# Performance work log

Measured on AMD Instinct MI355X. Metric: run time of the kernel, lower is better.

The kernel has to match this reference:

```python
import jax, jax.numpy as jnp
import numpy as np
from jax import lax

E = 8      # embed dim
H = 8      # num heads (head_dim = 1)
EPS = 1e-5


def pe_row(pos, d=E):
    # PositionalEncoding quirk: original adds pe[:, x.size(1), :] -> a SINGLE row at index L.
    i = jnp.arange(0, d, 2, dtype=jnp.float32)
    div = jnp.exp(i * (-np.log(10000.0) / d))
    row = jnp.zeros((d,), jnp.float32)
    row = row.at[0::2].set(jnp.sin(pos * div))
    row = row.at[1::2].set(jnp.cos(pos * div))
    return row


def layernorm(x, g, b):
    mu = jnp.mean(x, axis=-1, keepdims=True)
    var = jnp.mean((x - mu) ** 2, axis=-1, keepdims=True)
    return (x - mu) / jnp.sqrt(var + EPS) * g + b


def mha(q, k, v, wi, bi, wo, bo):
    # torch nn.MultiheadAttention, batch_first, eval mode (dropout off)
    d = E // H
    qp = q @ wi[:E].T + bi[:E]
    kp = k @ wi[E:2 * E].T + bi[E:2 * E]
    vp = v @ wi[2 * E:].T + bi[2 * E:]
    sh = lambda x: x.reshape(x.shape[0], x.shape[1], H, d).transpose(0, 2, 1, 3)
    qh, kh, vh = sh(qp), sh(kp), sh(vp)
    scores = jnp.einsum('bhqd,bhkd->bhqk', qh, kh) / np.sqrt(d)
    attn = jax.nn.softmax(scores, axis=-1)
    o = jnp.einsum('bhqk,bhkd->bhqd', attn, vh)
    B, _, L, _ = o.shape
    o = o.transpose(0, 2, 1, 3).reshape(B, L, E)
    return o @ wo.T + bo


def conv1d_k1p1(x, w, b):
    # Conv1d kernel_size=1, padding=1 (conv_tgt branch), then permute to (B, L, C)
    y = lax.conv_general_dilated(x, w, (1,), [(1, 1)],
                                 dimension_numbers=('NCW', 'OIW', 'NCW'))
    return (y + b[None, :, None]).transpose(0, 2, 1)


def setup_inputs() -> dict:
    key = jax.random.key(0)
    ks = jax.random.split(key, 32)
    B = 8192
    r = lambda i, shape, s=0.05: jax.random.normal(ks[i], shape, jnp.float32) * s
    return {
        'eeg': jax.random.normal(ks[0], (B, 2, 20, 118), jnp.float32),
        'pupil': jax.random.normal(ks[1], (B, 2, 30), jnp.float32),
        'speech': jax.random.normal(ks[2], (B, 2, 30), jnp.float32),
        'action': jax.random.normal(ks[3], (B, 2, 30), jnp.float32),
        'location': jax.random.normal(ks[4], (B, 3, 30), jnp.float32),
        'tgt': jax.random.normal(ks[5], (B, 30), jnp.float32),
        'eeg_conv_w': r(6, (E, 2, 20, 2), 0.1), 'eeg_conv_b': r(7, (E,)),
        'psa_conv_w': r(8, (E, 2, 1), 0.3), 'psa_conv_b': r(9, (E,)),
        'loc_conv_w': r(10, (E, 3, 1), 0.3), 'loc_conv_b': r(11, (E,)),
        'tgt_conv_w': r(12, (E, 1, 1), 0.3), 'tgt_conv_b': r(13, (E,)),
        'norm_g': jnp.ones((E,), jnp.float32), 'norm_b': jnp.zeros((E,), jnp.float32),
        'cross_in_w': r(14, (3 * E, E), 0.3), 'cross_in_b': r(15, (3 * E,)),
        'cross_out_w': r(16, (E, E), 0.3), 'cross_out_b': r(17, (E,)),
        'self_in_w': r(18, (3 * E, E), 0.3), 'self_in_b': r(19, (3 * E,)),
        'self_out_w': r(20, (E, E), 0.3), 'self_out_b': r(21, (E,)),
        'out_in_w': r(22, (3 * E, E), 0.3), 'out_in_b': r(23, (3 * E,)),
        'out_out_w': r(24, (E, E), 0.3), 'out_out_b': r(25, (E,)),
        'fc1_w': r(26, (90, 256), 0.1), 'fc1_b': r(27, (90,)),
    }


def reference(eeg, pupil, speech, action, location, tgt,
              eeg_conv_w, eeg_conv_b, psa_conv_w, psa_conv_b,
              loc_conv_w, loc_conv_b, tgt_conv_w, tgt_conv_b,
              norm_g, norm_b,
              cross_in_w, cross_in_b, cross_out_w, cross_out_b,
              self_in_w, self_in_b, self_out_w, self_out_b,
              out_in_w, out_in_b, out_out_w, out_out_b,
              fc1_w, fc1_b):
    B = eeg.shape[0]
    # eeg conv2d: (B,2,20,118) -> (B,8,1,30) -> (B,30,8)
    e = lax.conv_general_dilated(eeg, eeg_conv_w, (1, 4), 'VALID',
                                 dimension_numbers=('NCHW', 'OIHW', 'NCHW'))
    e = (e + eeg_conv_b[None, :, None, None]).squeeze(2).transpose(0, 2, 1)
    # pupil/speech/action/location (raw len 30 -> conv_tgt branch -> seq 32)
    p = conv1d_k1p1(pupil, psa_conv_w, psa_conv_b)
    s = conv1d_k1p1(speech, psa_conv_w, psa_conv_b)
    a = conv1d_k1p1(action, psa_conv_w, psa_conv_b)
    l = conv1d_k1p1(location, loc_conv_w, loc_conv_b)
    # positional encoding adds single row pe[L]
    e = e + pe_row(30.0)
    p = p + pe_row(32.0)
    s = s + pe_row(32.0)
    a = a + pe_row(32.0)
    l = l + pe_row(32.0)

    cross = lambda q, kv: mha(q, kv, kv, cross_in_w, cross_in_b, cross_out_w, cross_out_b)
    selfa = lambda x: mha(x, x, x, self_in_w, self_in_b, self_out_w, self_out_b)
    nrm = lambda x: layernorm(x, norm_g, norm_b)

    eeg_final = (nrm(cross(e, p)) + nrm(cross(e, a)) + nrm(cross(e, l))
                 + nrm(selfa(e)) + nrm(cross(e, s)))
    pupil_final = (nrm(cross(p, e)) + nrm(cross(p, a)) + nrm(cross(p, l))
                   + nrm(selfa(p)) + nrm(cross(p, s)))
    s_cross_l = nrm(cross(s, l))
    speech_final = (nrm(cross(s, e)) + nrm(cross(s, p)) + nrm(cross(s, a))
                    + s_cross_l)  # original omits speech_self
    # original bug: action_cross_location = norm(speech_cross_location)
    action_final = (nrm(cross(a, e)) + nrm(cross(a, p)) + s_cross_l
                    + nrm(selfa(a)) + nrm(cross(a, s)))
    concatenated = jnp.concatenate([eeg_final, pupil_final, action_final, speech_final], axis=1)  # (B,126,8)

    t = conv1d_k1p1(tgt[:, None, :], tgt_conv_w, tgt_conv_b)  # (B,32,8)
    t = t + pe_row(32.0)
    out = mha(t, concatenated, concatenated, out_in_w, out_in_b, out_out_w, out_out_b)  # (B,32,8)
    out = out.reshape(B, 32 * E) @ fc1_w.T + fc1_b  # (B,90)
    out = out.reshape(B, 30, 3).transpose(0, 2, 1)  # (B,3,30)
    return jax.nn.softmax(out, axis=1)
```

## Files before the change

kernel.cpp:

```cpp
#include <hip/hip_runtime.h>
#include <cstdint>
#include <cstddef>

#define NT 256
#define LOG2E 1.4426950408889634f

typedef float v2f __attribute__((ext_vector_type(2)));
typedef float v4f __attribute__((ext_vector_type(4)));

#if defined(__has_builtin)
#  if __has_builtin(__builtin_amdgcn_exp2f)
#    define EXP2F(x) __builtin_amdgcn_exp2f(x)
#  else
#    define EXP2F(x) exp2f(x)
#  endif
#else
#  define EXP2F(x) exp2f(x)
#endif

enum {
  OFF_EEGB = 0,
  OFF_PSAW = 8,
  OFF_PSAB = 24,
  OFF_LOCW = 32,
  OFF_LOCB = 56,
  OFF_TGTW = 64,
  OFF_TGTB = 72,
  OFF_NG   = 80,
  OFF_NB   = 88,
  OFF_CINW = 96,
  OFF_CINB = 288,
  OFF_COUTW= 312,
  OFF_COUTB= 376,
  OFF_SINW = 384,
  OFF_SINB = 576,
  OFF_SOUTW= 600,
  OFF_SOUTB= 664,
  OFF_OINW = 672,
  OFF_OINB = 864,
  OFF_OOUTW= 888,
  OFF_OOUTB= 952,
  OFF_FC1B = 960,
  OFF_PE30 = 1052,
  OFF_PE32 = 1060,
  OFF_Ebuf = 1068,
  OFF_Pbuf = 1308,
  OFF_Sbuf = 1564,
  OFF_Abuf = 1820,
  OFF_Lbuf = 2076,
  OFF_Tbuf = 2332,
  OFF_CAT  = 2588,
  OFF_QP   = 3596,
  OFF_K8   = 4236,
  OFF_V8   = 6540,
  OFF_FCO  = 8844,
  SM_TOTAL = 8936,
  OFF_EEGW = OFF_K8,
  OFF_KF   = OFF_K8,
  OFF_VF   = OFF_K8 + 1056,
};


__device__ __forceinline__ float grp8_sum(float v) {
  v += __shfl_xor(v, 1);
  v += __shfl_xor(v, 2);
  v += __shfl_xor(v, 4);
  return v;
}

__device__ __forceinline__ float dot8(const float* __restrict__ x,
                                      const float* __restrict__ w, float bias) {
  v4f xa = *(const v4f*)x, xb = *(const v4f*)(x + 4);
  v4f p = xa * *(const v4f*)w;
  p += xb * *(const v4f*)(w + 4);
  v2f q = p.xy + p.zw;
  return bias + q.x + q.y;
}

template<int LK>
__device__ __forceinline__ void kvproj(int set, int src, int winO, int binO,
                                       float* __restrict__ sm, int tid) {
  if (tid < LK * 8) {
    int r = tid >> 3, hh = tid & 7;
    const float* x = sm + src + r * 8;
    float kk = dot8(x, sm + winO + 64 + hh * 8, sm[binO + 8 + hh]);
    float vv = dot8(x, sm + winO + 128 + hh * 8, sm[binO + 16 + hh]);
    sm[OFF_K8 + set * 288 + hh * 36 + r] = kk;
    sm[OFF_V8 + set * 288 + hh * 36 + r] = vv;
  }
}

template<int LK>
__device__ __forceinline__ float attn_nv(float q, int qi, int h, int set,
                                         int woutO, int boutO, float* __restrict__ sm) {
  const float* Kp = sm + OFF_K8 + set * 288 + h * 36;
  const float* Vp = sm + OFF_V8 + set * 288 + h * 36;
  v4f l4 = {0.f,0.f,0.f,0.f}, A4 = {0.f,0.f,0.f,0.f};
  #pragma unroll
  for (int t = 0; t < (LK >> 2); t++) {
    v4f kk = *(const v4f*)(Kp + 4 * t);
    v4f vv = *(const v4f*)(Vp + 4 * t);
    v4f sc = kk * q;
    v4f ee = { EXP2F(sc.x), EXP2F(sc.y), EXP2F(sc.z), EXP2F(sc.w) };
    l4 += ee; A4 += ee * vv;
  }
  if constexpr ((LK & 3) != 0) {
    v2f kk = *(const v2f*)(Kp + (LK & ~3));
    v2f vv = *(const v2f*)(Vp + (LK & ~3));
    v2f sc = kk * q;
    v2f ee = { EXP2F(sc.x), EXP2F(sc.y) };
    l4.xy = l4.xy + ee; A4.xy = A4.xy + ee * vv;
  }
  v2f lp = l4.xy + l4.zw, ap = A4.xy + A4.zw;
  float ov = (ap.x + ap.y) * __builtin_amdgcn_rcpf(lp.x + lp.y);
  sm[OFF_QP + qi * 20 + h] = ov;
  float a = dot8(sm + OFF_QP + qi * 20, sm + woutO + h * 8, sm[boutO + h]);
  float mu = grp8_sum(a) * 0.125f;
  float dd = a - mu;
  return fmaf(dd * rsqrtf(grp8_sum(dd * dd) * 0.125f + 1e-5f),
              sm[OFF_NG + h], sm[OFF_NB + h]);
}

__global__ __launch_bounds__(NT, 4) void cmt_kernel(
    const float* __restrict__ eeg, const float* __restrict__ pupil,
    const float* __restrict__ speech, const float* __restrict__ action,
    const float* __restrict__ location, const float* __restrict__ tgt,
    const float* __restrict__ eeg_w, const float* __restrict__ eeg_b,
    const float* __restrict__ psa_w, const float* __restrict__ psa_b,
    const float* __restrict__ loc_w, const float* __restrict__ loc_b,
    const float* __restrict__ tgt_w, const float* __restrict__ tgt_b,
    const float* __restrict__ ng, const float* __restrict__ nb,
    const float* __restrict__ cin_w, const float* __restrict__ cin_b,
    const float* __restrict__ cout_w, const float* __restrict__ cout_b,
    const float* __restrict__ sin_w, const float* __restrict__ sin_b,
    const float* __restrict__ sout_w, const float* __restrict__ sout_b,
    const float* __restrict__ oin_w, const float* __restrict__ oin_b,
    const float* __restrict__ oout_w, const float* __restrict__ oout_b,
    const float* __restrict__ fc1_w, const float* __restrict__ fc1_b,
    float* __restrict__ out)
{
  __shared__ __align__(16) float sm[SM_TOTAL];
  const int tid = threadIdx.x;
  const int b = blockIdx.x;

#define CP(off, p, n) for (int i = tid; i < (n); i += NT) sm[(off)+i] = (p)[i]
#define CPQ(off, p, n, nq) for (int i = tid; i < (n); i += NT) sm[(off)+i] = (p)[i] * ((i < (nq)) ? LOG2E : 1.0f)

  for (int i = tid; i < 640; i += NT) sm[OFF_EEGW + (i / 80) * 84 + (i % 80)] = eeg_w[i];
  CP(OFF_EEGB, eeg_b, 8);
  CP(OFF_PSAW, psa_w, 16);   CP(OFF_PSAB, psa_b, 8);
  CP(OFF_LOCW, loc_w, 24);   CP(OFF_LOCB, loc_b, 8);
  CP(OFF_TGTW, tgt_w, 8);    CP(OFF_TGTB, tgt_b, 8);
  CP(OFF_NG, ng, 8);         CP(OFF_NB, nb, 8);
  CPQ(OFF_CINW, cin_w, 192, 64);  CPQ(OFF_CINB, cin_b, 24, 8);
  CP(OFF_COUTW, cout_w, 64); CP(OFF_COUTB, cout_b, 8);
  CPQ(OFF_SINW, sin_w, 192, 64);  CPQ(OFF_SINB, sin_b, 24, 8);
  CP(OFF_SOUTW, sout_w, 64); CP(OFF_SOUTB, sout_b, 8);
  CPQ(OFF_OINW, oin_w, 192, 64);  CPQ(OFF_OINB, oin_b, 24, 8);
  CP(OFF_OOUTW, oout_w, 64); CP(OFF_OOUTB, oout_b, 8);
  CP(OFF_FC1B, fc1_b, 90);
  if (tid < 16) {
    const float divs[4] = {1.f, 0.1f, 0.01f, 0.001f};
    float pos = (tid < 8) ? 30.f : 32.f;
    int e = tid & 7;
    float x = pos * divs[e >> 1];
    float v = (e & 1) ? cosf(x) : sinf(x);
    sm[((tid < 8) ? OFF_PE30 : OFF_PE32) + e] = v;
  }
  __syncthreads();

  if (tid < 240) {
    int w = tid >> 3, o = tid & 7;
    const float* ep = eeg + (size_t)b * 4720 + 4 * w;
    const float* wr = sm + OFF_EEGW + o * 84;
    v4f acc4 = {0.f, 0.f, 0.f, 0.f};
    #pragma unroll
    for (int t = 0; t < 20; t++) {
      int ik0 = 2 * t, ik1 = 2 * t + 1;
      float2 x0 = *(const float2*)(ep + (ik0 / 20) * 2360 + (ik0 % 20) * 118);
      float2 x1 = *(const float2*)(ep + (ik1 / 20) * 2360 + (ik1 % 20) * 118);
      v4f xv = {x0.x, x0.y, x1.x, x1.y};
      acc4 += xv * *(const v4f*)(wr + 4 * t);
    }
    v2f s2 = acc4.xy + acc4.zw;
    sm[OFF_Ebuf + w * 8 + o] = s2.x + s2.y + sm[OFF_EEGB + o] + sm[OFF_PE30 + o];
  }
  {
    int t = tid >> 3, o = tid & 7;
    bool inb = (t >= 1 && t <= 30);
    int ti = t - 1;
    float pe = sm[OFF_PE32 + o];
    float w0 = sm[OFF_PSAW + 2 * o], w1 = sm[OFF_PSAW + 2 * o + 1];
    float pb = sm[OFF_PSAB + o];
    float vp = pb, vs = pb, va = pb;
    float vl = sm[OFF_LOCB + o], vt = sm[OFF_TGTB + o];
    if (inb) {
      const float* pp = pupil    + (size_t)b * 60 + ti;
      const float* sp = speech   + (size_t)b * 60 + ti;
      const float* ap = action   + (size_t)b * 60 + ti;
      const float* lp = location + (size_t)b * 90 + ti;
      vp = fmaf(pp[0], w0, fmaf(pp[30], w1, vp));
      vs = fmaf(sp[0], w0, fmaf(sp[30], w1, vs));
      va = fmaf(ap[0], w0, fmaf(ap[30], w1, va));
      vl = fmaf(lp[0],  sm[OFF_LOCW + 3 * o],     vl);
      vl = fmaf(lp[30], sm[OFF_LOCW + 3 * o + 1], vl);
      vl = fmaf(lp[60], sm[OFF_LOCW + 3 * o + 2], vl);
      vt = fmaf(tgt[(size_t)b * 30 + ti], sm[OFF_TGTW + o], vt);
    }
    sm[OFF_Pbuf + tid] = vp + pe;
    sm[OFF_Sbuf + tid] = vs + pe;
    sm[OFF_Abuf + tid] = va + pe;
    sm[OFF_Lbuf + tid] = vl + pe;
    sm[OFF_Tbuf + tid] = vt + pe;
  }
  __syncthreads();

  kvproj<30>(0, OFF_Ebuf, OFF_CINW, OFF_CINB, sm, tid);
  kvproj<32>(1, OFF_Pbuf, OFF_CINW, OFF_CINB, sm, tid);
  kvproj<32>(2, OFF_Sbuf, OFF_CINW, OFF_CINB, sm, tid);
  kvproj<32>(3, OFF_Abuf, OFF_CINW, OFF_CINB, sm, tid);
  kvproj<32>(4, OFF_Lbuf, OFF_CINW, OFF_CINB, sm, tid);
  kvproj<30>(5, OFF_Ebuf, OFF_SINW, OFF_SINB, sm, tid);
  kvproj<32>(6, OFF_Pbuf, OFF_SINW, OFF_SINB, sm, tid);
  kvproj<32>(7, OFF_Abuf, OFF_SINW, OFF_SINB, sm, tid);
  __syncthreads();

  const int qi = tid >> 3, h = tid & 7;
  float carry;
  {
    if (qi < 30) {
      const float* xr = sm + OFF_Ebuf + qi * 8;
      float qc = dot8(xr, sm + OFF_CINW + h * 8, sm[OFF_CINB + h]);
      float qs = dot8(xr, sm + OFF_SINW + h * 8, sm[OFF_SINB + h]);
      float cat = attn_nv<32>(qc, qi, h, 1, OFF_COUTW, OFF_COUTB, sm)
                + attn_nv<32>(qc, qi, h, 3, OFF_COUTW, OFF_COUTB, sm)
                + attn_nv<32>(qc, qi, h, 4, OFF_COUTW, OFF_COUTB, sm)
                + attn_nv<30>(qs, qi, h, 5, OFF_SOUTW, OFF_SOUTB, sm)
                + attn_nv<32>(qc, qi, h, 2, OFF_COUTW, OFF_COUTB, sm);
      sm[OFF_CAT + qi * 8 + h] = cat;
    }
    {
      const float* xr = sm + OFF_Pbuf + qi * 8;
      float qc = dot8(xr, sm + OFF_CINW + h * 8, sm[OFF_CINB + h]);
      float qs = dot8(xr, sm + OFF_SINW + h * 8, sm[OFF_SINB + h]);
      float cat = attn_nv<30>(qc, qi, h, 0, OFF_COUTW, OFF_COUTB, sm)
                + attn_nv<32>(qc, qi, h, 3, OFF_COUTW, OFF_COUTB, sm)
                + attn_nv<32>(qc, qi, h, 4, OFF_COUTW, OFF_COUTB, sm)
                + attn_nv<32>(qs, qi, h, 6, OFF_SOUTW, OFF_SOUTB, sm)
                + attn_nv<32>(qc, qi, h, 2, OFF_COUTW, OFF_COUTB, sm);
      sm[OFF_CAT + (30 + qi) * 8 + h] = cat;
    }
    {
      const float* xr = sm + OFF_Sbuf + qi * 8;
      float qc = dot8(xr, sm + OFF_CINW + h * 8, sm[OFF_CINB + h]);
      float n1 = attn_nv<30>(qc, qi, h, 0, OFF_COUTW, OFF_COUTB, sm);
      float n2 = attn_nv<32>(qc, qi, h, 1, OFF_COUTW, OFF_COUTB, sm);
      float n3 = attn_nv<32>(qc, qi, h, 3, OFF_COUTW, OFF_COUTB, sm);
      carry    = attn_nv<32>(qc, qi, h, 4, OFF_COUTW, OFF_COUTB, sm);
      sm[OFF_CAT + (94 + qi) * 8 + h] = n1 + n2 + n3 + carry;
    }
    {
      const float* xr = sm + OFF_Abuf + qi * 8;
      float qc = dot8(xr, sm + OFF_CINW + h * 8, sm[OFF_CINB + h]);
      float qs = dot8(xr, sm + OFF_SINW + h * 8, sm[OFF_SINB + h]);
      float cat = attn_nv<30>(qc, qi, h, 0, OFF_COUTW, OFF_COUTB, sm)
                + attn_nv<32>(qc, qi, h, 1, OFF_COUTW, OFF_COUTB, sm)
                + carry
                + attn_nv<32>(qs, qi, h, 7, OFF_SOUTW, OFF_SOUTB, sm)
                + attn_nv<32>(qc, qi, h, 2, OFF_COUTW, OFF_COUTB, sm);
      sm[OFF_CAT + (62 + qi) * 8 + h] = cat;
    }
  }
  __syncthreads();

  for (int j = tid; j < 1008; j += NT) {
    int r = j >> 3, hh = j & 7;
    const float* x = sm + OFF_CAT + r * 8;
    float kk = dot8(x, sm + OFF_OINW + 64 + hh * 8, sm[OFF_OINB + 8 + hh]);
    float vv = dot8(x, sm + OFF_OINW + 128 + hh * 8, sm[OFF_OINB + 16 + hh]);
    sm[OFF_KF + hh * 132 + r] = kk;
    sm[OFF_VF + hh * 132 + r] = vv;
  }
  __syncthreads();

  {
    float qf = dot8(sm + OFF_Tbuf + qi * 8, sm + OFF_OINW + h * 8, sm[OFF_OINB + h]);
    const float* Kp = sm + OFF_KF + h * 132;
    const float* Vp = sm + OFF_VF + h * 132;
    v4f l4 = {0.f,0.f,0.f,0.f}, A4 = {0.f,0.f,0.f,0.f};
    #pragma unroll
    for (int t = 0; t < 31; t++) {
      v4f kk = *(const v4f*)(Kp + 4 * t);
      v4f vv = *(const v4f*)(Vp + 4 * t);
      v4f sc = kk * qf;
      v4f ee = { EXP2F(sc.x), EXP2F(sc.y), EXP2F(sc.z), EXP2F(sc.w) };
      l4 += ee; A4 += ee * vv;
    }
    {
      v2f kk = *(const v2f*)(Kp + 124);
      v2f vv = *(const v2f*)(Vp + 124);
      v2f sc = kk * qf;
      v2f ee = { EXP2F(sc.x), EXP2F(sc.y) };
      l4.xy = l4.xy + ee; A4.xy = A4.xy + ee * vv;
    }
    v2f lp = l4.xy + l4.zw, ap = A4.xy + A4.zw;
    float ov = (ap.x + ap.y) * __builtin_amdgcn_rcpf(lp.x + lp.y);
    sm[OFF_QP + qi * 20 + h] = ov;
    float a = dot8(sm + OFF_QP + qi * 20, sm + OFF_OOUTW + h * 8, sm[OFF_OOUTB + h]);
    sm[OFF_Tbuf + qi * 8 + h] = a;
  }
  __syncthreads();

  if (tid < 180) {
    int j = tid >> 1, p = tid & 1;
    const v4f* w4 = (const v4f*)(fc1_w + j * 256);
    const v4f* o4 = (const v4f*)(sm + OFF_Tbuf);
    v4f acc4 = {0.f, 0.f, 0.f, 0.f};
    #pragma unroll 8
    for (int c = p; c < 64; c += 2) acc4 += o4[c] * w4[c];
    v2f a2 = acc4.xy + acc4.zw;
    float acc = a2.x + a2.y;
    acc += __shfl_xor(acc, 1);
    if (p == 0) sm[OFF_FCO + j] = acc + sm[OFF_FC1B + j];
  }
  __syncthreads();
  if (tid < 30) {
    float x0 = sm[OFF_FCO + 3 * tid], x1 = sm[OFF_FCO + 3 * tid + 1], x2 = sm[OFF_FCO + 3 * tid + 2];
    float m = fmaxf(x0, fmaxf(x1, x2));
    float e0 = __expf(x0 - m), e1 = __expf(x1 - m), e2 = __expf(x2 - m);
    float inv = __builtin_amdgcn_rcpf(e0 + e1 + e2);
    float* op = out + (size_t)b * 90;
    op[tid]      = e0 * inv;
    op[30 + tid] = e1 * inv;
    op[60 + tid] = e2 * inv;
  }
#undef CP
#undef CPQ
}

extern "C" void kernel_launch(void* const* d_in, const int* in_sizes, int n_in,
                              void* d_out, int out_size, void* d_ws, size_t ws_size,
                              hipStream_t stream) {
  (void)n_in; (void)out_size; (void)d_ws; (void)ws_size;
  int B = in_sizes[0] / 4720;
  cmt_kernel<<<B, NT, 0, stream>>>(
      (const float*)d_in[0],  (const float*)d_in[1],  (const float*)d_in[2],
      (const float*)d_in[3],  (const float*)d_in[4],  (const float*)d_in[5],
      (const float*)d_in[6],  (const float*)d_in[7],  (const float*)d_in[8],
      (const float*)d_in[9],  (const float*)d_in[10], (const float*)d_in[11],
      (const float*)d_in[12], (const float*)d_in[13], (const float*)d_in[14],
      (const float*)d_in[15], (const float*)d_in[16], (const float*)d_in[17],
      (const float*)d_in[18], (const float*)d_in[19], (const float*)d_in[20],
      (const float*)d_in[21], (const float*)d_in[22], (const float*)d_in[23],
      (const float*)d_in[24], (const float*)d_in[25], (const float*)d_in[26],
      (const float*)d_in[27], (const float*)d_in[28], (const float*)d_in[29],
      (float*)d_out);
}
```

Baseline: 251.0 us.

## Split cross/self K/V projection phases to shrink LDS and use shuffles for out-proj

Reduces shared memory from 8936 to 6476 floats by computing cross-attention K/V sets first, then reusing the same buffer for the self-attention K/V sets in a second phase, and raising launch bounds from 4 to 6 blocks. The per-head attention output is now exchanged through lane shuffles instead of a store to an LDS scratch row followed by a reload, which removes the QP buffer. Projection weights are hoisted into registers per thread. The cost is extra barriers and a read-modify-write pass on the concatenated buffer, plus higher register pressure under the tighter launch bound.

Result: slower. 260.3 us (+3.7%).

```diff
diff --git a/kernel.cpp b/kernel.cpp
--- a/kernel.cpp
+++ b/kernel.cpp
@@ -50,16 +50,19 @@
   OFF_Lbuf = 2076,
   OFF_Tbuf = 2332,
   OFF_CAT  = 2588,
-  OFF_QP   = 3596,
-  OFF_K8   = 4236,
-  OFF_V8   = 6540,
-  OFF_FCO  = 8844,
-  SM_TOTAL = 8936,
-  OFF_EEGW = OFF_K8,
-  OFF_KF   = OFF_K8,
-  OFF_VF   = OFF_K8 + 1056,
+  OFF_KV   = 3596,
+  SM_TOTAL = 6476,
+  OFF_KVV  = OFF_KV + 1440,
+  OFF_EEGW = OFF_KV,
+  OFF_KF   = OFF_KV,
+  OFF_VF   = OFF_KV + 1056,
+  OFF_FCO  = OFF_KV + 2112,
 };
 
+__device__ __forceinline__ float hsum4(v4f a) {
+  v2f t = a.xy + a.zw;
+  return t.x + t.y;
+}
 
 __device__ __forceinline__ float grp8_sum(float v) {
   v += __shfl_xor(v, 1);
@@ -71,30 +74,14 @@
 __device__ __forceinline__ float dot8(const float* __restrict__ x,
                                       const float* __restrict__ w, float bias) {
   v4f xa = *(const v4f*)x, xb = *(const v4f*)(x + 4);
-  v4f p = xa * *(const v4f*)w;
-  p += xb * *(const v4f*)(w + 4);
-  v2f q = p.xy + p.zw;
-  return bias + q.x + q.y;
+  return bias + hsum4(xa * *(const v4f*)w + xb * *(const v4f*)(w + 4));
 }
 
 template<int LK>
-__device__ __forceinline__ void kvproj(int set, int src, int winO, int binO,
-                                       float* __restrict__ sm, int tid) {
-  if (tid < LK * 8) {
-    int r = tid >> 3, hh = tid & 7;
-    const float* x = sm + src + r * 8;
-    float kk = dot8(x, sm + winO + 64 + hh * 8, sm[binO + 8 + hh]);
-    float vv = dot8(x, sm + winO + 128 + hh * 8, sm[binO + 16 + hh]);
-    sm[OFF_K8 + set * 288 + hh * 36 + r] = kk;
-    sm[OFF_V8 + set * 288 + hh * 36 + r] = vv;
-  }
-}
-
-template<int LK>
-__device__ __forceinline__ float attn_nv(float q, int qi, int h, int set,
-                                         int woutO, int boutO, float* __restrict__ sm) {
-  const float* Kp = sm + OFF_K8 + set * 288 + h * 36;
-  const float* Vp = sm + OFF_V8 + set * 288 + h * 36;
+__device__ __forceinline__ float attn_nv(float q, int h,
+                                         const float* Kp, const float* Vp,
+                                         const float* sm, int woutO, int boutO,
+                                         float gg, float bb) {
   v4f l4 = {0.f,0.f,0.f,0.f}, A4 = {0.f,0.f,0.f,0.f};
   #pragma unroll
   for (int t = 0; t < (LK >> 2); t++) {
@@ -111,17 +98,26 @@
     v2f ee = { EXP2F(sc.x), EXP2F(sc.y) };
     l4.xy = l4.xy + ee; A4.xy = A4.xy + ee * vv;
   }
-  v2f lp = l4.xy + l4.zw, ap = A4.xy + A4.zw;
-  float ov = (ap.x + ap.y) * __builtin_amdgcn_rcpf(lp.x + lp.y);
-  sm[OFF_QP + qi * 20 + h] = ov;
-  float a = dot8(sm + OFF_QP + qi * 20, sm + woutO + h * 8, sm[boutO + h]);
+  float ov = hsum4(A4) * __builtin_amdgcn_rcpf(hsum4(l4));
+  int lb = (threadIdx.x & 63) & ~7;
+  v4f woa = *(const v4f*)(sm + woutO + h * 8);
+  v4f wob = *(const v4f*)(sm + woutO + h * 8 + 4);
+  float a = sm[boutO + h];
+  a = fmaf(__shfl(ov, lb + 0), woa.x, a);
+  a = fmaf(__shfl(ov, lb + 1), woa.y, a);
+  a = fmaf(__shfl(ov, lb + 2), woa.z, a);
+  a = fmaf(__shfl(ov, lb + 3), woa.w, a);
+  a = fmaf(__shfl(ov, lb + 4), wob.x, a);
+  a = fmaf(__shfl(ov, lb + 5), wob.y, a);
+  a = fmaf(__shfl(ov, lb + 6), wob.z, a);
+  a = fmaf(__shfl(ov, lb + 7), wob.w, a);
   float mu = grp8_sum(a) * 0.125f;
   float dd = a - mu;
-  return fmaf(dd * rsqrtf(grp8_sum(dd * dd) * 0.125f + 1e-5f),
-              sm[OFF_NG + h], sm[OFF_NB + h]);
-}
-
-__global__ __launch_bounds__(NT, 4) void cmt_kernel(
+  float var = grp8_sum(dd * dd) * 0.125f;
+  return fmaf(dd * rsqrtf(var + 1e-5f), gg, bb);
+}
+
+__global__ __launch_bounds__(NT, 6) void cmt_kernel(
     const float* __restrict__ eeg, const float* __restrict__ pupil,
     const float* __restrict__ speech, const float* __restrict__ action,
     const float* __restrict__ location, const float* __restrict__ tgt,
@@ -182,8 +178,7 @@
       v4f xv = {x0.x, x0.y, x1.x, x1.y};
       acc4 += xv * *(const v4f*)(wr + 4 * t);
     }
-    v2f s2 = acc4.xy + acc4.zw;
-    sm[OFF_Ebuf + w * 8 + o] = s2.x + s2.y + sm[OFF_EEGB + o] + sm[OFF_PE30 + o];
+    sm[OFF_Ebuf + w * 8 + o] = hsum4(acc4) + sm[OFF_EEGB + o] + sm[OFF_PE30 + o];
   }
   {
     int t = tid >> 3, o = tid & 7;
@@ -215,71 +210,113 @@
   }
   __syncthreads();
 
-  kvproj<30>(0, OFF_Ebuf, OFF_CINW, OFF_CINB, sm, tid);
-  kvproj<32>(1, OFF_Pbuf, OFF_CINW, OFF_CINB, sm, tid);
-  kvproj<32>(2, OFF_Sbuf, OFF_CINW, OFF_CINB, sm, tid);
-  kvproj<32>(3, OFF_Abuf, OFF_CINW, OFF_CINB, sm, tid);
-  kvproj<32>(4, OFF_Lbuf, OFF_CINW, OFF_CINB, sm, tid);
-  kvproj<30>(5, OFF_Ebuf, OFF_SINW, OFF_SINB, sm, tid);
-  kvproj<32>(6, OFF_Pbuf, OFF_SINW, OFF_SINB, sm, tid);
-  kvproj<32>(7, OFF_Abuf, OFF_SINW, OFF_SINB, sm, tid);
-  __syncthreads();
-
   const int qi = tid >> 3, h = tid & 7;
-  float carry;
-  {
+
+  {
+    const int r = qi;
+    v4f cka = *(const v4f*)(sm + OFF_CINW + 64 + h * 8), ckb = *(const v4f*)(sm + OFF_CINW + 68 + h * 8);
+    v4f cva = *(const v4f*)(sm + OFF_CINW + 128 + h * 8), cvb = *(const v4f*)(sm + OFF_CINW + 132 + h * 8);
+    float cbk = sm[OFF_CINB + 8 + h], cbv = sm[OFF_CINB + 16 + h];
+#define KV1(srcO, set) { \
+    v4f xa = *(const v4f*)(sm + (srcO) + r * 8); \
+    v4f xb = *(const v4f*)(sm + (srcO) + r * 8 + 4); \
+    sm[OFF_KV  + (set) * 288 + h * 36 + r] = cbk + hsum4(xa * cka + xb * ckb); \
+    sm[OFF_KVV + (set) * 288 + h * 36 + r] = cbv + hsum4(xa * cva + xb * cvb); }
+    if (r < 30) KV1(OFF_Ebuf, 0);
+    KV1(OFF_Pbuf, 1);
+    KV1(OFF_Sbuf, 2);
+    KV1(OFF_Abuf, 3);
+    KV1(OFF_Lbuf, 4);
+#undef KV1
+  }
+  __syncthreads();
+
+#define KSET(s) (sm + OFF_KV  + (s) * 288 + h * 36)
+#define VSET(s) (sm + OFF_KVV + (s) * 288 + h * 36)
+  {
+    const float gg = sm[OFF_NG + h], bb = sm[OFF_NB + h];
+    float carry;
     if (qi < 30) {
-      const float* xr = sm + OFF_Ebuf + qi * 8;
-      float qc = dot8(xr, sm + OFF_CINW + h * 8, sm[OFF_CINB + h]);
-      float qs = dot8(xr, sm + OFF_SINW + h * 8, sm[OFF_SINB + h]);
-      float cat = attn_nv<32>(qc, qi, h, 1, OFF_COUTW, OFF_COUTB, sm)
-                + attn_nv<32>(qc, qi, h, 3, OFF_COUTW, OFF_COUTB, sm)
-                + attn_nv<32>(qc, qi, h, 4, OFF_COUTW, OFF_COUTB, sm)
-                + attn_nv<30>(qs, qi, h, 5, OFF_SOUTW, OFF_SOUTB, sm)
-                + attn_nv<32>(qc, qi, h, 2, OFF_COUTW, OFF_COUTB, sm);
+      float qc = dot8(sm + OFF_Ebuf + qi * 8, sm + OFF_CINW + h * 8, sm[OFF_CINB + h]);
+      float cat = attn_nv<32>(qc, h, KSET(1), VSET(1), sm, OFF_COUTW, OFF_COUTB, gg, bb)
+                + attn_nv<32>(qc, h, KSET(3), VSET(3), sm, OFF_COUTW, OFF_COUTB, gg, bb)
+                + attn_nv<32>(qc, h, KSET(4), VSET(4), sm, OFF_COUTW, OFF_COUTB, gg, bb)
+                + attn_nv<32>(qc, h, KSET(2), VSET(2), sm, OFF_COUTW, OFF_COUTB, gg, bb);
       sm[OFF_CAT + qi * 8 + h] = cat;
     }
     {
-      const float* xr = sm + OFF_Pbuf + qi * 8;
-      float qc = dot8(xr, sm + OFF_CINW + h * 8, sm[OFF_CINB + h]);
-      float qs = dot8(xr, sm + OFF_SINW + h * 8, sm[OFF_SINB + h]);
-      float cat = attn_nv<30>(qc, qi, h, 0, OFF_COUTW, OFF_COUTB, sm)
-                + attn_nv<32>(qc, qi, h, 3, OFF_COUTW, OFF_COUTB, sm)
-                + attn_nv<32>(qc, qi, h, 4, OFF_COUTW, OFF_COUTB, sm)
-                + attn_nv<32>(qs, qi, h, 6, OFF_SOUTW, OFF_SOUTB, sm)
-                + attn_nv<32>(qc, qi, h, 2, OFF_COUTW, OFF_COUTB, sm);
+      float qc = dot8(sm + OFF_Pbuf + qi * 8, sm + OFF_CINW + h * 8, sm[OFF_CINB + h]);
+      float cat = attn_nv<30>(qc, h, KSET(0), VSET(0), sm, OFF_COUTW, OFF_COUTB, gg, bb)
+                + attn_nv<32>(qc, h, KSET(3), VSET(3), sm, OFF_COUTW, OFF_COUTB, gg, bb)
+                + attn_nv<32>(qc, h, KSET(4), VSET(4), sm, OFF_COUTW, OFF_COUTB, gg, bb)
+                + attn_nv<32>(qc, h, KSET(2), VSET(2), sm, OFF_COUTW, OFF_COUTB, gg, bb);
       sm[OFF_CAT + (30 + qi) * 8 + h] = cat;
     }
     {
-      const float* xr = sm + OFF_Sbuf + qi * 8;
-      float qc = dot8(xr, sm + OFF_CINW + h * 8, sm[OFF_CINB + h]);
-      float n1 = attn_nv<30>(qc, qi, h, 0, OFF_COUTW, OFF_COUTB, sm);
-      float n2 = attn_nv<32>(qc, qi, h, 1, OFF_COUTW, OFF_COUTB, sm);
-      float n3 = attn_nv<32>(qc, qi, h, 3, OFF_COUTW, OFF_COUTB, sm);
-      carry    = attn_nv<32>(qc, qi, h, 4, OFF_COUTW, OFF_COUTB, sm);
-      sm[OFF_CAT + (94 + qi) * 8 + h] = n1 + n2 + n3 + carry;
-    }
-    {
-      const float* xr = sm + OFF_Abuf + qi * 8;
-      float qc = dot8(xr, sm + OFF_CINW + h * 8, sm[OFF_CINB + h]);
-      float qs = dot8(xr, sm + OFF_SINW + h * 8, sm[OFF_SINB + h]);
-      float cat = attn_nv<30>(qc, qi, h, 0, OFF_COUTW, OFF_COUTB, sm)
-                + attn_nv<32>(qc, qi, h, 1, OFF_COUTW, OFF_COUTB, sm)
-                + carry
-                + attn_nv<32>(qs, qi, h, 7, OFF_SOUTW, OFF_SOUTB, sm)
-                + attn_nv<32>(qc, qi, h, 2, OFF_COUTW, OFF_COUTB, sm);
+      float qc = dot8(sm + OFF_Sbuf + qi * 8, sm + OFF_CINW + h * 8, sm[OFF_CINB + h]);
+      float cat = attn_nv<30>(qc, h, KSET(0), VSET(0), sm, OFF_COUTW, OFF_COUTB, gg, bb)
+                + attn_nv<32>(qc, h, KSET(1), VSET(1), sm, OFF_COUTW, OFF_COUTB, gg, bb)
+                + attn_nv<32>(qc, h, KSET(3), VSET(3), sm, OFF_COUTW, OFF_COUTB, gg, bb);
+      carry     = attn_nv<32>(qc, h, KSET(4), VSET(4), sm, OFF_COUTW, OFF_COUTB, gg, bb);
+      sm[OFF_CAT + (94 + qi) * 8 + h] = cat + carry;
+    }
+    {
+      float qc = dot8(sm + OFF_Abuf + qi * 8, sm + OFF_CINW + h * 8, sm[OFF_CINB + h]);
+      float cat = attn_nv<30>(qc, h, KSET(0), VSET(0), sm, OFF_COUTW, OFF_COUTB, gg, bb)
+                + attn_nv<32>(qc, h, KSET(1), VSET(1), sm, OFF_COUTW, OFF_COUTB, gg, bb)
+                + attn_nv<32>(qc, h, KSET(2), VSET(2), sm, OFF_COUTW, OFF_COUTB, gg, bb)
+                + carry;
       sm[OFF_CAT + (62 + qi) * 8 + h] = cat;
     }
   }
   __syncthreads();
 
-  for (int j = tid; j < 1008; j += NT) {
-    int r = j >> 3, hh = j & 7;
-    const float* x = sm + OFF_CAT + r * 8;
-    float kk = dot8(x, sm + OFF_OINW + 64 + hh * 8, sm[OFF_OINB + 8 + hh]);
-    float vv = dot8(x, sm + OFF_OINW + 128 + hh * 8, sm[OFF_OINB + 16 + hh]);
-    sm[OFF_KF + hh * 132 + r] = kk;
-    sm[OFF_VF + hh * 132 + r] = vv;
+  {
+    const int r = qi;
+    v4f ska = *(const v4f*)(sm + OFF_SINW + 64 + h * 8), skb = *(const v4f*)(sm + OFF_SINW + 68 + h * 8);
+    v4f sva = *(const v4f*)(sm + OFF_SINW + 128 + h * 8), svb = *(const v4f*)(sm + OFF_SINW + 132 + h * 8);
+    float sbk = sm[OFF_SINB + 8 + h], sbv = sm[OFF_SINB + 16 + h];
+#define KV1(srcO, set) { \
+    v4f xa = *(const v4f*)(sm + (srcO) + r * 8); \
+    v4f xb = *(const v4f*)(sm + (srcO) + r * 8 + 4); \
+    sm[OFF_KV  + (set) * 288 + h * 36 + r] = sbk + hsum4(xa * ska + xb * skb); \
+    sm[OFF_KVV + (set) * 288 + h * 36 + r] = sbv + hsum4(xa * sva + xb * svb); }
+    if (r < 30) KV1(OFF_Ebuf, 0);
+    KV1(OFF_Pbuf, 1);
+    KV1(OFF_Abuf, 2);
+#undef KV1
+  }
+  __syncthreads();
+
+  {
+    const float gg = sm[OFF_NG + h], bb = sm[OFF_NB + h];
+    if (qi < 30) {
+      float qs = dot8(sm + OFF_Ebuf + qi * 8, sm + OFF_SINW + h * 8, sm[OFF_SINB + h]);
+      sm[OFF_CAT + qi * 8 + h] += attn_nv<30>(qs, h, KSET(0), VSET(0), sm, OFF_SOUTW, OFF_SOUTB, gg, bb);
+    }
+    {
+      float qs = dot8(sm + OFF_Pbuf + qi * 8, sm + OFF_SINW + h * 8, sm[OFF_SINB + h]);
+      sm[OFF_CAT + (30 + qi) * 8 + h] += attn_nv<32>(qs, h, KSET(1), VSET(1), sm, OFF_SOUTW, OFF_SOUTB, gg, bb);
+    }
+    {
+      float qs = dot8(sm + OFF_Abuf + qi * 8, sm + OFF_SINW + h * 8, sm[OFF_SINB + h]);
+      sm[OFF_CAT + (62 + qi) * 8 + h] += attn_nv<32>(qs, h, KSET(2), VSET(2), sm, OFF_SOUTW, OFF_SOUTB, gg, bb);
+    }
+  }
+#undef KSET
+#undef VSET
+  __syncthreads();
+
+  {
+    v4f fka = *(const v4f*)(sm + OFF_OINW + 64 + h * 8), fkb = *(const v4f*)(sm + OFF_OINW + 68 + h * 8);
+    v4f fva = *(const v4f*)(sm + OFF_OINW + 128 + h * 8), fvb = *(const v4f*)(sm + OFF_OINW + 132 + h * 8);
+    float fbk = sm[OFF_OINB + 8 + h], fbv = sm[OFF_OINB + 16 + h];
+    for (int r = qi; r < 126; r += 32) {
+      v4f xa = *(const v4f*)(sm + OFF_CAT + r * 8);
+      v4f xb = *(const v4f*)(sm + OFF_CAT + r * 8 + 4);
+      sm[OFF_KF + h * 132 + r] = fbk + hsum4(xa * fka + xb * fkb);
+      sm[OFF_VF + h * 132 + r] = fbv + hsum4(xa * fva + xb * fvb);
+    }
   }
   __syncthreads();
 
@@ -303,10 +340,20 @@
       v2f ee = { EXP2F(sc.x), EXP2F(sc.y) };
       l4.xy = l4.xy + ee; A4.xy = A4.xy + ee * vv;
     }
-    v2f lp = l4.xy + l4.zw, ap = A4.xy + A4.zw;
-    float ov = (ap.x + ap.y) * __builtin_amdgcn_rcpf(lp.x + lp.y);
-    sm[OFF_QP + qi * 20 + h] = ov;
-    float a = dot8(sm + OFF_QP + qi * 20, sm + OFF_OOUTW + h * 8, sm[OFF_OOUTB + h]);
+    float ov = hsum4(A4) * __builtin_amdgcn_rcpf(hsum4(l4));
+    int lb = (tid & 63) & ~7;
+    v4f woa = *(const v4f*)(sm + OFF_OOUTW + h * 8);
+    v4f wob = *(const v4f*)(sm + OFF_OOUTW + h * 8 + 4);
+    float a = sm[OFF_OOUTB + h];
+    a = fmaf(__shfl(ov, lb + 0), woa.x, a);
+    a = fmaf(__shfl(ov, lb + 1), woa.y, a);
+    a = fmaf(__shfl(ov, lb + 2), woa.z, a);
+    a = fmaf(__shfl(ov, lb + 3), woa.w, a);
+    a = fmaf(__shfl(ov, lb + 4), wob.x, a);
+    a = fmaf(__shfl(ov, lb + 5), wob.y, a);
+    a = fmaf(__shfl(ov, lb + 6), wob.z, a);
+    a = fmaf(__shfl(ov, lb + 7), wob.w, a);
+    __syncthreads();
     sm[OFF_Tbuf + qi * 8 + h] = a;
   }
   __syncthreads();
@@ -318,8 +365,7 @@
     v4f acc4 = {0.f, 0.f, 0.f, 0.f};
     #pragma unroll 8
     for (int c = p; c < 64; c += 2) acc4 += o4[c] * w4[c];
-    v2f a2 = acc4.xy + acc4.zw;
-    float acc = a2.x + a2.y;
+    float acc = hsum4(acc4);
     acc += __shfl_xor(acc, 1);
     if (p == 0) sm[OFF_FCO + j] = acc + sm[OFF_FC1B + j];
   }
```

## Table-drive attention blocks in a rolled loop and compute layernorm via LDS

Applied to the files above, without the earlier changes.

Replaces the 18 fully inlined attention calls with a rolled loop over a constant-memory descriptor table, which shrinks code size and register pressure. Layernorm statistics are now computed by writing to and reading back the per-query LDS slot instead of using cross-lane shuffles. KV projection weights are hoisted into registers across the source sets. The rolled loop adds descriptor loads, branching, and a runtime choice between the 30 and 32 key lengths.

Measured after the change: 276.1 us. 1.1x slower.

```diff
diff --git a/kernel.cpp b/kernel.cpp
--- a/kernel.cpp
+++ b/kernel.cpp
@@ -60,41 +60,43 @@
   OFF_VF   = OFF_K8 + 1056,
 };
 
-
-__device__ __forceinline__ float grp8_sum(float v) {
-  v += __shfl_xor(v, 1);
-  v += __shfl_xor(v, 2);
-  v += __shfl_xor(v, 4);
-  return v;
+struct BD { short qoff, Lq, set, sel, dst, flags; };
+static __device__ const BD g_bd[18] = {
+  {OFF_Ebuf, 30, 1, 0,  0, 1},
+  {OFF_Ebuf, 30, 3, 0,  0, 0},
+  {OFF_Ebuf, 30, 4, 0,  0, 0},
+  {OFF_Ebuf, 30, 5, 1,  0, 0},
+  {OFF_Ebuf, 30, 2, 0,  0, 2},
+  {OFF_Pbuf, 32, 0, 0, 30, 1},
+  {OFF_Pbuf, 32, 3, 0, 30, 0},
+  {OFF_Pbuf, 32, 4, 0, 30, 0},
+  {OFF_Pbuf, 32, 6, 1, 30, 0},
+  {OFF_Pbuf, 32, 2, 0, 30, 2},
+  {OFF_Sbuf, 32, 0, 0, 94, 1},
+  {OFF_Sbuf, 32, 1, 0, 94, 0},
+  {OFF_Sbuf, 32, 3, 0, 94, 0},
+  {OFF_Sbuf, 32, 4, 0, 94, 2|4},
+  {OFF_Abuf, 32, 0, 0, 62, 1},
+  {OFF_Abuf, 32, 1, 0, 62, 0},
+  {OFF_Abuf, 32, 2, 0, 62, 0},
+  {OFF_Abuf, 32, 7, 1, 62, 2|8},
+};
+
+__device__ __forceinline__ float hsum4(v4f a) {
+  v2f t = a.xy + a.zw;
+  return t.x + t.y;
 }
 
 __device__ __forceinline__ float dot8(const float* __restrict__ x,
                                       const float* __restrict__ w, float bias) {
   v4f xa = *(const v4f*)x, xb = *(const v4f*)(x + 4);
-  v4f p = xa * *(const v4f*)w;
-  p += xb * *(const v4f*)(w + 4);
-  v2f q = p.xy + p.zw;
-  return bias + q.x + q.y;
+  return bias + hsum4(xa * *(const v4f*)w + xb * *(const v4f*)(w + 4));
 }
 
 template<int LK>
-__device__ __forceinline__ void kvproj(int set, int src, int winO, int binO,
-                                       float* __restrict__ sm, int tid) {
-  if (tid < LK * 8) {
-    int r = tid >> 3, hh = tid & 7;
-    const float* x = sm + src + r * 8;
-    float kk = dot8(x, sm + winO + 64 + hh * 8, sm[binO + 8 + hh]);
-    float vv = dot8(x, sm + winO + 128 + hh * 8, sm[binO + 16 + hh]);
-    sm[OFF_K8 + set * 288 + hh * 36 + r] = kk;
-    sm[OFF_V8 + set * 288 + hh * 36 + r] = vv;
-  }
-}
-
-template<int LK>
-__device__ __forceinline__ float attn_nv(float q, int qi, int h, int set,
-                                         int woutO, int boutO, float* __restrict__ sm) {
-  const float* Kp = sm + OFF_K8 + set * 288 + h * 36;
-  const float* Vp = sm + OFF_V8 + set * 288 + h * 36;
+__device__ __forceinline__ float attn1_nv(float q, const float* Kp, const float* Vp,
+                                          float* qslot, int h, const float* sm,
+                                          int woutO, int boutO, float gg, float bb) {
   v4f l4 = {0.f,0.f,0.f,0.f}, A4 = {0.f,0.f,0.f,0.f};
   #pragma unroll
   for (int t = 0; t < (LK >> 2); t++) {
@@ -111,14 +113,17 @@
     v2f ee = { EXP2F(sc.x), EXP2F(sc.y) };
     l4.xy = l4.xy + ee; A4.xy = A4.xy + ee * vv;
   }
-  v2f lp = l4.xy + l4.zw, ap = A4.xy + A4.zw;
-  float ov = (ap.x + ap.y) * __builtin_amdgcn_rcpf(lp.x + lp.y);
-  sm[OFF_QP + qi * 20 + h] = ov;
-  float a = dot8(sm + OFF_QP + qi * 20, sm + woutO + h * 8, sm[boutO + h]);
-  float mu = grp8_sum(a) * 0.125f;
-  float dd = a - mu;
-  return fmaf(dd * rsqrtf(grp8_sum(dd * dd) * 0.125f + 1e-5f),
-              sm[OFF_NG + h], sm[OFF_NB + h]);
+  float ov = hsum4(A4) * __builtin_amdgcn_rcpf(hsum4(l4));
+  qslot[h] = ov;
+  v4f c0 = *(const v4f*)qslot, c1 = *(const v4f*)(qslot + 4);
+  v4f woa = *(const v4f*)(sm + woutO + h * 8), wob = *(const v4f*)(sm + woutO + h * 8 + 4);
+  float a = sm[boutO + h] + hsum4(c0 * woa + c1 * wob);
+  qslot[h] = a;
+  c0 = *(const v4f*)qslot; c1 = *(const v4f*)(qslot + 4);
+  float mu = hsum4(c0 + c1) * 0.125f;
+  v4f e0 = c0 - mu, e1 = c1 - mu;
+  float var = hsum4(e0 * e0 + e1 * e1) * 0.125f;
+  return fmaf((a - mu) * rsqrtf(var + 1e-5f), gg, bb);
 }
 
 __global__ __launch_bounds__(NT, 4) void cmt_kernel(
@@ -182,8 +187,7 @@
       v4f xv = {x0.x, x0.y, x1.x, x1.y};
       acc4 += xv * *(const v4f*)(wr + 4 * t);
     }
-    v2f s2 = acc4.xy + acc4.zw;
-    sm[OFF_Ebuf + w * 8 + o] = s2.x + s2.y + sm[OFF_EEGB + o] + sm[OFF_PE30 + o];
+    sm[OFF_Ebuf + w * 8 + o] = hsum4(acc4) + sm[OFF_EEGB + o] + sm[OFF_PE30 + o];
   }
   {
     int t = tid >> 3, o = tid & 7;
@@ -215,71 +219,71 @@
   }
   __syncthreads();
 
-  kvproj<30>(0, OFF_Ebuf, OFF_CINW, OFF_CINB, sm, tid);
-  kvproj<32>(1, OFF_Pbuf, OFF_CINW, OFF_CINB, sm, tid);
-  kvproj<32>(2, OFF_Sbuf, OFF_CINW, OFF_CINB, sm, tid);
-  kvproj<32>(3, OFF_Abuf, OFF_CINW, OFF_CINB, sm, tid);
-  kvproj<32>(4, OFF_Lbuf, OFF_CINW, OFF_CINB, sm, tid);
-  kvproj<30>(5, OFF_Ebuf, OFF_SINW, OFF_SINB, sm, tid);
-  kvproj<32>(6, OFF_Pbuf, OFF_SINW, OFF_SINB, sm, tid);
-  kvproj<32>(7, OFF_Abuf, OFF_SINW, OFF_SINB, sm, tid);
-  __syncthreads();
-
   const int qi = tid >> 3, h = tid & 7;
-  float carry;
-  {
-    if (qi < 30) {
-      const float* xr = sm + OFF_Ebuf + qi * 8;
-      float qc = dot8(xr, sm + OFF_CINW + h * 8, sm[OFF_CINB + h]);
-      float qs = dot8(xr, sm + OFF_SINW + h * 8, sm[OFF_SINB + h]);
-      float cat = attn_nv<32>(qc, qi, h, 1, OFF_COUTW, OFF_COUTB, sm)
-                + attn_nv<32>(qc, qi, h, 3, OFF_COUTW, OFF_COUTB, sm)
-                + attn_nv<32>(qc, qi, h, 4, OFF_COUTW, OFF_COUTB, sm)
-                + attn_nv<30>(qs, qi, h, 5, OFF_SOUTW, OFF_SOUTB, sm)
-                + attn_nv<32>(qc, qi, h, 2, OFF_COUTW, OFF_COUTB, sm);
-      sm[OFF_CAT + qi * 8 + h] = cat;
-    }
-    {
-      const float* xr = sm + OFF_Pbuf + qi * 8;
-      float qc = dot8(xr, sm + OFF_CINW + h * 8, sm[OFF_CINB + h]);
-      float qs = dot8(xr, sm + OFF_SINW + h * 8, sm[OFF_SINB + h]);
-      float cat = attn_nv<30>(qc, qi, h, 0, OFF_COUTW, OFF_COUTB, sm)
-                + attn_nv<32>(qc, qi, h, 3, OFF_COUTW, OFF_COUTB, sm)
-                + attn_nv<32>(qc, qi, h, 4, OFF_COUTW, OFF_COUTB, sm)
-                + attn_nv<32>(qs, qi, h, 6, OFF_SOUTW, OFF_SOUTB, sm)
-                + attn_nv<32>(qc, qi, h, 2, OFF_COUTW, OFF_COUTB, sm);
-      sm[OFF_CAT + (30 + qi) * 8 + h] = cat;
-    }
-    {
-      const float* xr = sm + OFF_Sbuf + qi * 8;
-      float qc = dot8(xr, sm + OFF_CINW + h * 8, sm[OFF_CINB + h]);
-      float n1 = attn_nv<30>(qc, qi, h, 0, OFF_COUTW, OFF_COUTB, sm);
-      float n2 = attn_nv<32>(qc, qi, h, 1, OFF_COUTW, OFF_COUTB, sm);
-      float n3 = attn_nv<32>(qc, qi, h, 3, OFF_COUTW, OFF_COUTB, sm);
-      carry    = attn_nv<32>(qc, qi, h, 4, OFF_COUTW, OFF_COUTB, sm);
-      sm[OFF_CAT + (94 + qi) * 8 + h] = n1 + n2 + n3 + carry;
-    }
-    {
-      const float* xr = sm + OFF_Abuf + qi * 8;
-      float qc = dot8(xr, sm + OFF_CINW + h * 8, sm[OFF_CINB + h]);
-      float qs = dot8(xr, sm + OFF_SINW + h * 8, sm[OFF_SINB + h]);
-      float cat = attn_nv<30>(qc, qi, h, 0, OFF_COUTW, OFF_COUTB, sm)
-                + attn_nv<32>(qc, qi, h, 1, OFF_COUTW, OFF_COUTB, sm)
-                + carry
-                + attn_nv<32>(qs, qi, h, 7, OFF_SOUTW, OFF_SOUTB, sm)
-                + attn_nv<32>(qc, qi, h, 2, OFF_COUTW, OFF_COUTB, sm);
-      sm[OFF_CAT + (62 + qi) * 8 + h] = cat;
-    }
-  }
-  __syncthreads();
-
-  for (int j = tid; j < 1008; j += NT) {
-    int r = j >> 3, hh = j & 7;
-    const float* x = sm + OFF_CAT + r * 8;
-    float kk = dot8(x, sm + OFF_OINW + 64 + hh * 8, sm[OFF_OINB + 8 + hh]);
-    float vv = dot8(x, sm + OFF_OINW + 128 + hh * 8, sm[OFF_OINB + 16 + hh]);
-    sm[OFF_KF + hh * 132 + r] = kk;
-    sm[OFF_VF + hh * 132 + r] = vv;
+  float* qslot = sm + OFF_QP + qi * 20;
+
+  {
+    const int r = qi;
+    v4f cka = *(const v4f*)(sm + OFF_CINW + 64 + h * 8), ckb = *(const v4f*)(sm + OFF_CINW + 68 + h * 8);
+    v4f cva = *(const v4f*)(sm + OFF_CINW + 128 + h * 8), cvb = *(const v4f*)(sm + OFF_CINW + 132 + h * 8);
+    float cbk = sm[OFF_CINB + 8 + h], cbv = sm[OFF_CINB + 16 + h];
+#define KV1(srcO, set, wka, wkb, wva, wvb, bk, bv) { \
+    v4f xa = *(const v4f*)(sm + (srcO) + r * 8); \
+    v4f xb = *(const v4f*)(sm + (srcO) + r * 8 + 4); \
+    sm[OFF_K8 + (set) * 288 + h * 36 + r] = (bk) + hsum4(xa * (wka) + xb * (wkb)); \
+    sm[OFF_V8 + (set) * 288 + h * 36 + r] = (bv) + hsum4(xa * (wva) + xb * (wvb)); }
+    if (r < 30) KV1(OFF_Ebuf, 0, cka, ckb, cva, cvb, cbk, cbv);
+    KV1(OFF_Pbuf, 1, cka, ckb, cva, cvb, cbk, cbv);
+    KV1(OFF_Sbuf, 2, cka, ckb, cva, cvb, cbk, cbv);
+    KV1(OFF_Abuf, 3, cka, ckb, cva, cvb, cbk, cbv);
+    KV1(OFF_Lbuf, 4, cka, ckb, cva, cvb, cbk, cbv);
+    v4f ska = *(const v4f*)(sm + OFF_SINW + 64 + h * 8), skb = *(const v4f*)(sm + OFF_SINW + 68 + h * 8);
+    v4f sva = *(const v4f*)(sm + OFF_SINW + 128 + h * 8), svb = *(const v4f*)(sm + OFF_SINW + 132 + h * 8);
+    float sbk = sm[OFF_SINB + 8 + h], sbv = sm[OFF_SINB + 16 + h];
+    if (r < 30) KV1(OFF_Ebuf, 5, ska, skb, sva, svb, sbk, sbv);
+    KV1(OFF_Pbuf, 6, ska, skb, sva, svb, sbk, sbv);
+    KV1(OFF_Abuf, 7, ska, skb, sva, svb, sbk, sbv);
+#undef KV1
+  }
+  __syncthreads();
+
+  {
+    const float gg = sm[OFF_NG + h], bb = sm[OFF_NB + h];
+    float cat = 0.f, carry = 0.f;
+    #pragma unroll 1
+    for (int mi = 0; mi < 18; mi++) {
+      const BD d = g_bd[mi];
+      if (qi < d.Lq) {
+        const int winO  = d.sel ? OFF_SINW  : OFF_CINW;
+        const int binO  = d.sel ? OFF_SINB  : OFF_CINB;
+        const int woutO = d.sel ? OFF_SOUTW : OFF_COUTW;
+        const int boutO = d.sel ? OFF_SOUTB : OFF_COUTB;
+        float q = dot8(sm + d.qoff + qi * 8, sm + winO + h * 8, sm[binO + h]);
+        const float* Kp = sm + OFF_K8 + d.set * 288 + h * 36;
+        const float* Vp = sm + OFF_V8 + d.set * 288 + h * 36;
+        bool lk30 = (d.set == 0) | (d.set == 5);
+        float nv = lk30 ? attn1_nv<30>(q, Kp, Vp, qslot, h, sm, woutO, boutO, gg, bb)
+                        : attn1_nv<32>(q, Kp, Vp, qslot, h, sm, woutO, boutO, gg, bb);
+        if (d.flags & 1) cat = 0.f;
+        cat += nv;
+        if (d.flags & 4) carry = nv;
+        if (d.flags & 8) cat += carry;
+        if (d.flags & 2) sm[OFF_CAT + (d.dst + qi) * 8 + h] = cat;
+      }
+    }
+  }
+  __syncthreads();
+
+  {
+    v4f fka = *(const v4f*)(sm + OFF_OINW + 64 + h * 8), fkb = *(const v4f*)(sm + OFF_OINW + 68 + h * 8);
+    v4f fva = *(const v4f*)(sm + OFF_OINW + 128 + h * 8), fvb = *(const v4f*)(sm + OFF_OINW + 132 + h * 8);
+    float fbk = sm[OFF_OINB + 8 + h], fbv = sm[OFF_OINB + 16 + h];
+    for (int r = qi; r < 126; r += 32) {
+      v4f xa = *(const v4f*)(sm + OFF_CAT + r * 8);
+      v4f xb = *(const v4f*)(sm + OFF_CAT + r * 8 + 4);
+      sm[OFF_KF + h * 132 + r] = fbk + hsum4(xa * fka + xb * fkb);
+      sm[OFF_VF + h * 132 + r] = fbv + hsum4(xa * fva + xb * fvb);
+    }
   }
   __syncthreads();
 
@@ -303,10 +307,11 @@
       v2f ee = { EXP2F(sc.x), EXP2F(sc.y) };
       l4.xy = l4.xy + ee; A4.xy = A4.xy + ee * vv;
     }
-    v2f lp = l4.xy + l4.zw, ap = A4.xy + A4.zw;
-    float ov = (ap.x + ap.y) * __builtin_amdgcn_rcpf(lp.x + lp.y);
-    sm[OFF_QP + qi * 20 + h] = ov;
-    float a = dot8(sm + OFF_QP + qi * 20, sm + OFF_OOUTW + h * 8, sm[OFF_OOUTB + h]);
+    float ov = hsum4(A4) * __builtin_amdgcn_rcpf(hsum4(l4));
+    qslot[h] = ov;
+    v4f c0 = *(const v4f*)qslot, c1 = *(const v4f*)(qslot + 4);
+    v4f woa = *(const v4f*)(sm + OFF_OOUTW + h * 8), wob = *(const v4f*)(sm + OFF_OOUTW + h * 8 + 4);
+    float a = sm[OFF_OOUTB + h] + hsum4(c0 * woa + c1 * wob);
     sm[OFF_Tbuf + qi * 8 + h] = a;
   }
   __syncthreads();
@@ -318,8 +323,7 @@
     v4f acc4 = {0.f, 0.f, 0.f, 0.f};
     #pragma unroll 8
     for (int c = p; c < 64; c += 2) acc4 += o4[c] * w4[c];
-    v2f a2 = acc4.xy + acc4.zw;
-    float acc = a2.x + a2.y;
+    float acc = hsum4(acc4);
     acc += __shfl_xor(acc, 1);
     if (p == 0) sm[OFF_FCO + j] = acc + sm[OFF_FC1B + j];
   }
```
